# Kernel optimization log

Hardware: AMD Instinct MI355X
Metric: run time of the kernel (lower is better)

Reference implementation:

```python
import jax, jax.numpy as jnp
import numpy as np

CH = 8       # MASK_HEAD.HEAD_CHANNELS
IN_CH = 8    # MASK_BRANCH.OUT_CHANNELS
MASK_OUT_STRIDE = 4
SOI = jnp.array([64.0, 128.0, 256.0, 512.0, 1024.0], dtype=jnp.float32)


def _upsample_ac(x, factor, axis):
    # align_corners=True bilinear upsample along one axis: L -> factor*(L-1)+1
    L = x.shape[axis]
    M = factor * (L - 1) + 1
    pos = jnp.arange(M, dtype=jnp.float32) / factor
    i0 = jnp.floor(pos).astype(jnp.int32)
    i1 = jnp.minimum(i0 + 1, L - 1)
    frac = pos - i0.astype(jnp.float32)
    x0 = jnp.take(x, i0, axis=axis)
    x1 = jnp.take(x, i1, axis=axis)
    sh = [1] * x.ndim
    sh[axis] = M
    frac = frac.reshape(sh)
    return x0 * (1.0 - frac) + x1 * frac


def aligned_bilinear(x, factor):
    # x: [n, 1, H, W] -> [n, 1, factor*H, factor*W] (AdelaiDet aligned_bilinear)
    if factor == 1:
        return x
    h, w = x.shape[2], x.shape[3]
    x = jnp.pad(x, ((0, 0), (0, 0), (0, 1), (0, 1)), mode='edge')
    x = _upsample_ac(x, factor, 2)
    x = _upsample_ac(x, factor, 3)
    p = factor // 2
    x = jnp.pad(x, ((0, 0), (0, 0), (p, 0), (p, 0)), mode='edge')
    return x[:, :, :factor * h, :factor * w]


def setup_inputs() -> dict:
    key = jax.random.key(0)
    k1, k2, k3, k4, k5, k6 = jax.random.split(key, 6)
    N, H, W = 4, 128, 128
    n_inst = 400
    num_gen = (IN_CH + 2) * CH + CH + CH * CH + CH + CH * 1 + 1  # 169
    return {
        'mask_feats': jax.random.normal(k1, (N, IN_CH, H, W), dtype=jnp.float32),
        'mask_shift': jax.random.uniform(k2, (H * W, 2), dtype=jnp.float32),
        'shifts': jax.random.uniform(k3, (n_inst, 2), dtype=jnp.float32),
        'inst_params': jax.random.normal(k4, (n_inst, num_gen), dtype=jnp.float32),
        'im_inds': jax.random.randint(k5, (n_inst,), 0, N, dtype=jnp.int32),
        'fpn_levels': jax.random.randint(k6, (n_inst,), 0, 5, dtype=jnp.int32),
        'mask_feat_stride': 8,
    }


def reference(mask_feats, mask_shift, shifts, inst_params, im_inds, fpn_levels, mask_feat_stride):
    n = inst_params.shape[0]
    N, C, H, W = mask_feats.shape
    # relative coords: [n, 2, H*W]
    rel = shifts[:, None, :] - mask_shift[None, :, :]          # [n, HW, 2]
    rel = jnp.transpose(rel, (0, 2, 1))                        # [n, 2, HW]
    rel = rel / SOI[fpn_levels][:, None, None]
    feats = mask_feats[im_inds].reshape(n, C, H * W)           # [n, C, HW]
    x = jnp.concatenate([rel, feats], axis=1)                  # [n, C+2, HW]
    # parse dynamic params: weights first, then biases
    w1 = inst_params[:, 0:80].reshape(n, CH, IN_CH + 2)
    w2 = inst_params[:, 80:144].reshape(n, CH, CH)
    w3 = inst_params[:, 144:152].reshape(n, 1, CH)
    b1 = inst_params[:, 152:160]
    b2 = inst_params[:, 160:168]
    b3 = inst_params[:, 168:169]
    # per-instance 1x1 convs == batched tiny GEMMs
    x = jax.nn.relu(jnp.einsum('noc,ncp->nop', w1, x) + b1[:, :, None])
    x = jax.nn.relu(jnp.einsum('noc,ncp->nop', w2, x) + b2[:, :, None])
    x = jnp.einsum('noc,ncp->nop', w3, x) + b3[:, :, None]
    logits = x.reshape(n, 1, H, W)
    factor = int(mask_feat_stride) // MASK_OUT_STRIDE
    return aligned_bilinear(logits, factor)
```

## Files before the change

kernel.cpp:

```cpp
#include <hip/hip_runtime.h>


#define HW 16384
#define NP 169

__global__ __launch_bounds__(256, 8)
void dmh_kernel(const float* __restrict__ mask_feats,
                const float* __restrict__ mask_shift,
                const float* __restrict__ shifts,
                const float* __restrict__ inst_params,
                const int*   __restrict__ im_inds,
                const int*   __restrict__ fpn_levels,
                float*       __restrict__ out)
{
    __shared__ float lgE[576];
    __shared__ float lgO[576];

    const int bx   = blockIdx.x;
    const int inst = bx >> 4;
    const int rg   = bx & 15;
    const int tid  = threadIdx.x;
    const int r0   = rg * 8;

    const float* __restrict__ fb =
        mask_feats + (size_t)im_inds[inst] * 8 * HW;
    const float* __restrict__ wp = inst_params + (size_t)inst * NP;
    const float s0  = shifts[2 * inst];
    const float s1  = shifts[2 * inst + 1];
    const float inv = 1.0f / (float)(64 << fpn_levels[inst]);

    auto mlp_px = [&](int p) {
        const int t = p >> 7;
        const int c = p & 127;
        const int r = min(max(r0 - 1 + t, 0), 127);
        const int g = r * 128 + c;

        const float2 ms = *(const float2*)(mask_shift + 2 * g);
        const float x0 = (s0 - ms.x) * inv;
        const float x1 = (s1 - ms.y) * inv;
        float f[8];
        #pragma unroll
        for (int k = 0; k < 8; ++k) f[k] = fb[k * HW + g];

        float y1[8];
        #pragma unroll
        for (int o = 0; o < 8; ++o) {
            float a = wp[152 + o];
            a = fmaf(wp[o * 10], x0, a);
            a = fmaf(wp[o * 10 + 1], x1, a);
            #pragma unroll
            for (int k = 0; k < 8; ++k) a = fmaf(wp[o * 10 + 2 + k], f[k], a);
            y1[o] = fmaxf(a, 0.f);
        }
        float y2[8];
        #pragma unroll
        for (int o = 0; o < 8; ++o) {
            float a = wp[160 + o];
            #pragma unroll
            for (int k = 0; k < 8; ++k) a = fmaf(wp[80 + o * 8 + k], y1[k], a);
            y2[o] = fmaxf(a, 0.f);
        }
        float v = wp[168];
        #pragma unroll
        for (int k = 0; k < 8; ++k) v = fmaf(wp[144 + k], y2[k], v);

        const int idx = t * 64 + (c >> 1);
        if (c & 1) lgO[idx] = v; else lgE[idx] = v;
    };

    mlp_px(tid);
    mlp_px(tid + 256);
    mlp_px(tid + 512);
    mlp_px(tid + 768);
    if (tid < 128) mlp_px(tid + 1024);

    __syncthreads();

    float* __restrict__ op =
        out + (size_t)inst * 65536 + (size_t)(2 * r0) * 256;
    const int w = tid >> 6;
    const int l = tid & 63;

    #pragma unroll
    for (int j = 0; j < 4; ++j) {
        const int yl = w + 4 * j;
        float4 res;
        if (w & 1) {
            const int t0 = (yl + 1) >> 1;
            const float* e = lgE + t0 * 64;
            const float* o = lgO + t0 * 64;
            const float v0 = e[l];
            const float v1 = o[l];
            const float vm = (l > 0) ? o[l - 1] : v0;
            res = make_float4(0.5f * (vm + v0), v0, 0.5f * (v0 + v1), v1);
        } else {
            const int t0 = yl >> 1;
            const float* eA = lgE + t0 * 64;
            const float* oA = lgO + t0 * 64;
            const float* eB = eA + 64;
            const float* oB = oA + 64;
            const float v0A = eA[l], v1A = oA[l];
            const float v0B = eB[l], v1B = oB[l];
            const float vmA = (l > 0) ? oA[l - 1] : v0A;
            const float vmB = (l > 0) ? oB[l - 1] : v0B;
            const float hA0 = 0.5f * (vmA + v0A), hA2 = 0.5f * (v0A + v1A);
            const float hB0 = 0.5f * (vmB + v0B), hB2 = 0.5f * (v0B + v1B);
            res = make_float4(0.5f * (hA0 + hB0), 0.5f * (v0A + v0B),
                              0.5f * (hA2 + hB2), 0.5f * (v1A + v1B));
        }
        *(float4*)(op + yl * 256 + 4 * l) = res;
    }
}

extern "C" void kernel_launch(void* const* d_in, const int* in_sizes, int n_in,
                              void* d_out, int out_size, void* d_ws, size_t ws_size,
                              hipStream_t stream) {
    (void)n_in; (void)out_size; (void)d_ws; (void)ws_size;
    const float* mask_feats  = (const float*)d_in[0];
    const float* mask_shift  = (const float*)d_in[1];
    const float* shifts      = (const float*)d_in[2];
    const float* inst_params = (const float*)d_in[3];
    const int*   im_inds     = (const int*)d_in[4];
    const int*   fpn_levels  = (const int*)d_in[5];
    float* out = (float*)d_out;

    const int n_inst = in_sizes[2] / 2;
    dmh_kernel<<<dim3(n_inst * 16), dim3(256), 0, stream>>>(
        mask_feats, mask_shift, shifts, inst_params, im_inds, fpn_levels, out);
}
```

Before: 167.4 us.

## Repack mask features to pixel-major layout, process two pixels per thread, larger row tiles

Adds a pre-pass kernel that transposes mask_feats from channel-planar into pixel-interleaved records in workspace, so the main kernel loads 8 channels with two float4 loads instead of 8 strided loads. The main kernel now covers 16 output rows per block instead of 8, which cuts the duplicated halo-row MLP work, and computes two pixels per thread to share weight loads. It also lowers the occupancy hint. The cost is an extra launch plus a pass over the features, and the packed path only runs if the workspace is large enough.

```diff
diff --git a/kernel.cpp b/kernel.cpp
--- a/kernel.cpp
+++ b/kernel.cpp
@@ -4,75 +4,146 @@
 #define HW 16384
 #define NP 169
 
-__global__ __launch_bounds__(256, 8)
+__global__ __launch_bounds__(256)
+void pack_kernel(const float* __restrict__ mf, float* __restrict__ rec)
+{
+    const int g   = blockIdx.x * 256 + threadIdx.x;
+    const int img = g >> 14;
+    const int p   = g & 16383;
+    const float* fb = mf + (size_t)img * 8 * HW + p;
+    float4 a = make_float4(fb[0],      fb[HW],     fb[2 * HW], fb[3 * HW]);
+    float4 b = make_float4(fb[4 * HW], fb[5 * HW], fb[6 * HW], fb[7 * HW]);
+    float4* o = (float4*)(rec + (size_t)g * 8);
+    o[0] = a;
+    o[1] = b;
+}
+
+__global__ __launch_bounds__(256, 6)
 void dmh_kernel(const float* __restrict__ mask_feats,
                 const float* __restrict__ mask_shift,
                 const float* __restrict__ shifts,
                 const float* __restrict__ inst_params,
                 const int*   __restrict__ im_inds,
                 const int*   __restrict__ fpn_levels,
-                float*       __restrict__ out)
+                const float* __restrict__ rec,
+                float*       __restrict__ out,
+                int use_rec)
 {
-    __shared__ float lgE[576];
-    __shared__ float lgO[576];
+    __shared__ float lgE[17 * 64];
+    __shared__ float lgO[17 * 64];
 
     const int bx   = blockIdx.x;
-    const int inst = bx >> 4;
-    const int rg   = bx & 15;
+    const int inst = bx >> 3;
+    const int rg   = bx & 7;
     const int tid  = threadIdx.x;
-    const int r0   = rg * 8;
-
-    const float* __restrict__ fb =
-        mask_feats + (size_t)im_inds[inst] * 8 * HW;
+    const int r0   = rg * 16;
+
+    const int img = im_inds[inst];
     const float* __restrict__ wp = inst_params + (size_t)inst * NP;
     const float s0  = shifts[2 * inst];
     const float s1  = shifts[2 * inst + 1];
     const float inv = 1.0f / (float)(64 << fpn_levels[inst]);
-
-    auto mlp_px = [&](int p) {
+    const float* __restrict__ fb = mask_feats + (size_t)img * 8 * HW;
+    const float* __restrict__ rb = rec + (size_t)img * 8 * HW;
+
+    auto load_px = [&](int p, float* x) {
         const int t = p >> 7;
         const int c = p & 127;
         const int r = min(max(r0 - 1 + t, 0), 127);
         const int g = r * 128 + c;
-
         const float2 ms = *(const float2*)(mask_shift + 2 * g);
-        const float x0 = (s0 - ms.x) * inv;
-        const float x1 = (s1 - ms.y) * inv;
-        float f[8];
-        #pragma unroll
-        for (int k = 0; k < 8; ++k) f[k] = fb[k * HW + g];
-
-        float y1[8];
-        #pragma unroll
-        for (int o = 0; o < 8; ++o) {
-            float a = wp[152 + o];
-            a = fmaf(wp[o * 10], x0, a);
-            a = fmaf(wp[o * 10 + 1], x1, a);
-            #pragma unroll
-            for (int k = 0; k < 8; ++k) a = fmaf(wp[o * 10 + 2 + k], f[k], a);
-            y1[o] = fmaxf(a, 0.f);
-        }
-        float y2[8];
-        #pragma unroll
-        for (int o = 0; o < 8; ++o) {
-            float a = wp[160 + o];
-            #pragma unroll
-            for (int k = 0; k < 8; ++k) a = fmaf(wp[80 + o * 8 + k], y1[k], a);
-            y2[o] = fmaxf(a, 0.f);
-        }
-        float v = wp[168];
-        #pragma unroll
-        for (int k = 0; k < 8; ++k) v = fmaf(wp[144 + k], y2[k], v);
-
+        x[0] = (s0 - ms.x) * inv;
+        x[1] = (s1 - ms.y) * inv;
+        if (use_rec) {
+            const float4* q = (const float4*)(rb + (size_t)g * 8);
+            const float4 a = q[0], b = q[1];
+            x[2] = a.x; x[3] = a.y; x[4] = a.z; x[5] = a.w;
+            x[6] = b.x; x[7] = b.y; x[8] = b.z; x[9] = b.w;
+        } else {
+            #pragma unroll
+            for (int k = 0; k < 8; ++k) x[2 + k] = fb[k * HW + g];
+        }
+    };
+
+    auto store_px = [&](int p, float v) {
+        const int t = p >> 7;
+        const int c = p & 127;
         const int idx = t * 64 + (c >> 1);
         if (c & 1) lgO[idx] = v; else lgE[idx] = v;
     };
 
-    mlp_px(tid);
-    mlp_px(tid + 256);
-    mlp_px(tid + 512);
-    mlp_px(tid + 768);
-    if (tid < 128) mlp_px(tid + 1024);
+    #pragma unroll
+    for (int u = 0; u < 4; ++u) {
+        const int pA = tid + 512 * u;
+        const int pB = pA + 256;
+        float xa[10], xb[10];
+        load_px(pA, xa);
+        load_px(pB, xb);
+
+        float ya[8], yb[8];
+        #pragma unroll
+        for (int o = 0; o < 8; ++o) {
+            const float bia = wp[152 + o];
+            float a = bia, b = bia;
+            #pragma unroll
+            for (int c = 0; c < 10; ++c) {
+                const float w = wp[o * 10 + c];
+                a = fmaf(w, xa[c], a);
+                b = fmaf(w, xb[c], b);
+            }
+            ya[o] = fmaxf(a, 0.f);
+            yb[o] = fmaxf(b, 0.f);
+        }
+        float za[8], zb[8];
+        #pragma unroll
+        for (int o = 0; o < 8; ++o) {
+            const float bia = wp[160 + o];
+            float a = bia, b = bia;
+            #pragma unroll
+            for (int c = 0; c < 8; ++c) {
+                const float w = wp[80 + o * 8 + c];
+                a = fmaf(w, ya[c], a);
+                b = fmaf(w, yb[c], b);
+            }
+            za[o] = fmaxf(a, 0.f);
+            zb[o] = fmaxf(b, 0.f);
+        }
+        float va = wp[168], vb = va;
+        #pragma unroll
+        for (int c = 0; c < 8; ++c) {
+            const float w = wp[144 + c];
+            va = fmaf(w, za[c], va);
+            vb = fmaf(w, zb[c], vb);
+        }
+        store_px(pA, va);
+        store_px(pB, vb);
+    }
+
+    if (tid < 128) {
+        const int p = 2048 + tid;
+        float x[10];
+        load_px(p, x);
+        float y1[8];
+        #pragma unroll
+        for (int o = 0; o < 8; ++o) {
+            float a = wp[152 + o];
+            #pragma unroll
+            for (int c = 0; c < 10; ++c) a = fmaf(wp[o * 10 + c], x[c], a);
+            y1[o] = fmaxf(a, 0.f);
+        }
+        float y2[8];
+        #pragma unroll
+        for (int o = 0; o < 8; ++o) {
+            float a = wp[160 + o];
+            #pragma unroll
+            for (int c = 0; c < 8; ++c) a = fmaf(wp[80 + o * 8 + c], y1[c], a);
+            y2[o] = fmaxf(a, 0.f);
+        }
+        float v = wp[168];
+        #pragma unroll
+        for (int c = 0; c < 8; ++c) v = fmaf(wp[144 + c], y2[c], v);
+        store_px(p, v);
+    }
 
     __syncthreads();
 
@@ -80,33 +151,33 @@
         out + (size_t)inst * 65536 + (size_t)(2 * r0) * 256;
     const int w = tid >> 6;
     const int l = tid & 63;
+    const int parity = w & 1;
 
     #pragma unroll
-    for (int j = 0; j < 4; ++j) {
-        const int yl = w + 4 * j;
+    for (int j = 0; j < 8; ++j) {
+        const int p2 = (w >> 1) + 2 * j;
+        const int yl = 2 * p2 + parity;
         float4 res;
-        if (w & 1) {
-            const int t0 = (yl + 1) >> 1;
-            const float* e = lgE + t0 * 64;
-            const float* o = lgO + t0 * 64;
+        if (parity) {
+            const float* e = lgE + (p2 + 1) * 64;
+            const float* o = lgO + (p2 + 1) * 64;
             const float v0 = e[l];
             const float v1 = o[l];
             const float vm = (l > 0) ? o[l - 1] : v0;
             res = make_float4(0.5f * (vm + v0), v0, 0.5f * (v0 + v1), v1);
         } else {
-            const int t0 = yl >> 1;
-            const float* eA = lgE + t0 * 64;
-            const float* oA = lgO + t0 * 64;
+            const float* eA = lgE + p2 * 64;
+            const float* oA = lgO + p2 * 64;
             const float* eB = eA + 64;
             const float* oB = oA + 64;
             const float v0A = eA[l], v1A = oA[l];
             const float v0B = eB[l], v1B = oB[l];
             const float vmA = (l > 0) ? oA[l - 1] : v0A;
             const float vmB = (l > 0) ? oB[l - 1] : v0B;
-            const float hA0 = 0.5f * (vmA + v0A), hA2 = 0.5f * (v0A + v1A);
-            const float hB0 = 0.5f * (vmB + v0B), hB2 = 0.5f * (v0B + v1B);
-            res = make_float4(0.5f * (hA0 + hB0), 0.5f * (v0A + v0B),
-                              0.5f * (hA2 + hB2), 0.5f * (v1A + v1B));
+            res = make_float4(0.25f * (vmA + v0A + vmB + v0B),
+                              0.5f  * (v0A + v0B),
+                              0.25f * (v0A + v1A + v0B + v1B),
+                              0.5f  * (v1A + v1B));
         }
         *(float4*)(op + yl * 256 + 4 * l) = res;
     }
@@ -115,7 +186,7 @@
 extern "C" void kernel_launch(void* const* d_in, const int* in_sizes, int n_in,
                               void* d_out, int out_size, void* d_ws, size_t ws_size,
                               hipStream_t stream) {
-    (void)n_in; (void)out_size; (void)d_ws; (void)ws_size;
+    (void)n_in; (void)out_size;
     const float* mask_feats  = (const float*)d_in[0];
     const float* mask_shift  = (const float*)d_in[1];
     const float* shifts      = (const float*)d_in[2];
@@ -123,8 +194,17 @@
     const int*   im_inds     = (const int*)d_in[4];
     const int*   fpn_levels  = (const int*)d_in[5];
     float* out = (float*)d_out;
+    float* rec = (float*)d_ws;
 
     const int n_inst = in_sizes[2] / 2;
-    dmh_kernel<<<dim3(n_inst * 16), dim3(256), 0, stream>>>(
-        mask_feats, mask_shift, shifts, inst_params, im_inds, fpn_levels, out);
+    const size_t rec_bytes = (size_t)4 * HW * 8 * sizeof(float);
+    const int use_rec = (ws_size >= rec_bytes) ? 1 : 0;
+
+    if (use_rec)
+        pack_kernel<<<dim3(4 * HW / 256), dim3(256), 0, stream>>>(
+            mask_feats, rec);
+
+    dmh_kernel<<<dim3(n_inst * 8), dim3(256), 0, stream>>>(
+        mask_feats, mask_shift, shifts, inst_params, im_inds, fpn_levels,
+        rec, out, use_rec);
 }
```

Result: faster. 152.6 us (-8.8%).
